# Performance work log

Hardware: AMD Instinct MI355X
Metric: run time of the kernel (lower is better)

Reference implementation:

```python
import jax, jax.numpy as jnp
import numpy as np
import math

B, D, L = 32, 128, 512
NH = 8
DK = D // NH  # 16
DV = D // NH  # 16


def setup_inputs() -> dict:
    key = jax.random.key(0)
    kx, kq, kk, kv, ko = jax.random.split(key, 5)
    # xavier_normal std for [B, Dk, D] slabs: gain*sqrt(2/(fan_in+fan_out)) with fan over last two dims
    std_qkv = math.sqrt(2.0 / (DK + D))
    std_o = math.sqrt(2.0 / (DV * NH + D))
    x = jax.random.normal(kx, (B, D, L), dtype=jnp.float32)
    Wqs = jax.random.normal(kq, (NH, B, DK, D), dtype=jnp.float32) * std_qkv
    Wks = jax.random.normal(kk, (NH, B, DK, D), dtype=jnp.float32) * std_qkv
    Wvs = jax.random.normal(kv, (NH, B, DV, D), dtype=jnp.float32) * std_qkv
    Wo = jax.random.normal(ko, (B, DV * NH, D), dtype=jnp.float32) * std_o
    return {"x": x, "Wqs": Wqs, "Wks": Wks, "Wvs": Wvs, "Wo": Wo}


def reference(x, Wqs, Wks, Wvs, Wo):
    # x: [B, D, L]; Wqs/Wks: [NH, B, DK, D]; Wvs: [NH, B, DV, D]; Wo: [B, DV*NH, D]
    nh, b, dk, d = Wqs.shape
    l = x.shape[-1]
    inv_sqrt_dk = 1.0 / math.sqrt(dk)
    Q = jnp.einsum('nbkd,bdl->nbkl', Wqs, x)  # [NH, B, DK, L]
    K = jnp.einsum('nbkd,bdl->nbkl', Wks, x)  # [NH, B, DK, L]
    V = jnp.einsum('nbvd,bdl->nbvl', Wvs, x)  # [NH, B, DV, L]
    # scores[n,b,l,m] = sum_k Q[n,b,k,l]*K[n,b,k,m]; softmax over l (torch dim=1 of [B,L,L])
    scores = jnp.einsum('nbkl,nbkm->nblm', Q, K) * inv_sqrt_dk
    S = jax.nn.softmax(scores, axis=2)
    heads = jnp.einsum('nbvl,nblm->nbvm', V, S)  # [NH, B, DV, L]
    # .pop() in the original reverses head order before concatenation
    heads = heads[::-1]
    head = heads.transpose(1, 0, 2, 3).reshape(b, nh * heads.shape[2], l)  # [B, NH*DV, L]
    out = jnp.einsum('bod,bdl->bol', Wo, head)  # [B, D, L]
    return out
```

## Files before the change

### kernel.cpp

```cpp
#include <hip/hip_runtime.h>
#include <hip/hip_bf16.h>
#include <math.h>

#define B_   32
#define D_   128
#define L_   512
#define NH_  8
#define DK_  16

#define QKS  24
#define VST  520
#define XST  40

#define LOG2E 1.4426950408889634f
#define QSC   (0.25f * LOG2E)
#define SH2   (-11.541560327111707f)

typedef _Float16 h2 __attribute__((ext_vector_type(2)));
typedef _Float16 h4 __attribute__((ext_vector_type(4)));
typedef _Float16 h8 __attribute__((ext_vector_type(8)));
typedef __attribute__((ext_vector_type(4)))  float f32x4;
typedef __attribute__((ext_vector_type(16))) float f32x16;
typedef unsigned int u32x2 __attribute__((ext_vector_type(2)));
typedef unsigned int u32x4 __attribute__((ext_vector_type(4)));

__device__ __forceinline__ unsigned int cvt_pk_u(float a, float b) {
    return __builtin_bit_cast(unsigned int, __builtin_amdgcn_cvt_pkrtz(a, b));
}

#define MFMA_K32(a, b, c) __builtin_amdgcn_mfma_f32_16x16x32_f16((a), (b), (c), 0, 0, 0)
#define MFMA_32(a, b, c)  __builtin_amdgcn_mfma_f32_32x32x16_f16((a), (b), (c), 0, 0, 0)

__global__ __launch_bounds__(512, 2) void attn_mfma(
    const float* __restrict__ x,
    const float* __restrict__ Wq,
    const float* __restrict__ Wk,
    const float* __restrict__ Wv,
    _Float16* __restrict__ Ht)
{
    __shared__ __attribute__((aligned(16))) _Float16 T32[512 * XST];
    __shared__ __attribute__((aligned(16))) _Float16 Qh[512 * QKS];
    __shared__ __attribute__((aligned(16))) _Float16 Kh[512 * QKS];
    __shared__ __attribute__((aligned(16))) _Float16 Vs[32 * VST];

    const int nb = blockIdx.x;
    const int n  = nb >> 5;
    const int b  = nb & 31;
    const int t  = threadIdx.x;
    const int wv = t >> 6;
    const int ln = t & 63;
    const int l16 = ln & 15;
    const int g4  = ln >> 4;
    const int lm  = ln & 31;
    const int hi  = ln >> 5;

    const float* xb = x + (size_t)b * D_ * L_;
    const size_t woff = (size_t)(n * B_ + b) * DK_ * D_;
    const float* pWq = Wq + woff;
    const float* pWk = Wk + woff;
    const float* pWv = Wv + woff;

    {
        const h8 ones8 = {(_Float16)1.f,(_Float16)1.f,(_Float16)1.f,(_Float16)1.f,
                          (_Float16)1.f,(_Float16)1.f,(_Float16)1.f,(_Float16)1.f};
        #pragma unroll
        for (int i = 0; i < 2; ++i) {
            const int c = t + i * 512;
            const int row = 16 + (c >> 6), cc = (c & 63) * 8;
            *(h8*)&Vs[row * VST + cc] = ones8;
        }
    }

    const int sdd = (t >> 7) * 8;
    const int sl0 = (t & 127) * 4;

    f32x4 Qa[4], Ka[4], Va[4];
    #pragma unroll
    for (int lt = 0; lt < 4; ++lt) {
        Qa[lt] = (f32x4){0.f,0.f,0.f,0.f};
        Ka[lt] = (f32x4){0.f,0.f,0.f,0.f};
        Va[lt] = (f32x4){0.f,0.f,0.f,0.f};
    }

    for (int ks = 0; ks < 4; ++ks) {
        {
            f32x4 xv[8];
            #pragma unroll
            for (int j = 0; j < 8; ++j)
                xv[j] = *(const f32x4*)&xb[(size_t)(ks * 32 + sdd + j) * L_ + sl0];
            #pragma unroll
            for (int i = 0; i < 4; ++i) {
                h8 w;
                #pragma unroll
                for (int j = 0; j < 8; ++j) w[j] = (_Float16)xv[j][i];
                *(h8*)&T32[(sl0 + i) * XST + sdd] = w;
            }
        }
        __syncthreads();

        const int d0 = ks * 32 + g4 * 8;
        const float* aq = pWq + l16 * D_ + d0;
        const float* ak = pWk + l16 * D_ + d0;
        const float* av = pWv + l16 * D_ + d0;
        const f32x4 q0 = *(const f32x4*)aq, q1 = *(const f32x4*)(aq + 4);
        const f32x4 k0 = *(const f32x4*)ak, k1 = *(const f32x4*)(ak + 4);
        const f32x4 v0 = *(const f32x4*)av, v1 = *(const f32x4*)(av + 4);
        h8 Aq, Ak, Av;
        #pragma unroll
        for (int j = 0; j < 4; ++j) {
            Aq[j] = (_Float16)q0[j]; Aq[j + 4] = (_Float16)q1[j];
            Ak[j] = (_Float16)k0[j]; Ak[j + 4] = (_Float16)k1[j];
            Av[j] = (_Float16)v0[j]; Av[j + 4] = (_Float16)v1[j];
        }
        #pragma unroll
        for (int lt = 0; lt < 4; ++lt) {
            const int l = wv * 64 + lt * 16 + l16;
            const h8 Bx = *(const h8*)&T32[l * XST + g4 * 8];
            Qa[lt] = MFMA_K32(Aq, Bx, Qa[lt]);
            Ka[lt] = MFMA_K32(Ak, Bx, Ka[lt]);
            Va[lt] = MFMA_K32(Av, Bx, Va[lt]);
        }
        __syncthreads();
    }

    #pragma unroll
    for (int lt = 0; lt < 4; ++lt) {
        const int l = wv * 64 + lt * 16 + l16;
        h4 qv, kv;
        #pragma unroll
        for (int r = 0; r < 4; ++r) {
            qv[r] = (_Float16)(Qa[lt][r] * QSC);
            kv[r] = (_Float16)Ka[lt][r];
            Vs[(g4 * 4 + r) * VST + l] = (_Float16)Va[lt][r];
        }
        *(h4*)&Qh[l * QKS + g4 * 4] = qv;
        *(h4*)&Kh[l * QKS + g4 * 4] = kv;
    }
    __syncthreads();

    const int m0 = wv * 64;
    const h8 Bk0 = *(const h8*)&Kh[(m0 + lm) * QKS + 8 * hi];
    const h8 Bk1 = *(const h8*)&Kh[(m0 + 32 + lm) * QKS + 8 * hi];

    f32x16 shiftacc, pv0, pv1;
    #pragma unroll
    for (int i = 0; i < 16; ++i) { shiftacc[i] = SH2; pv0[i] = 0.f; pv1[i] = 0.f; }

    #pragma unroll 2
    for (int t32 = 0; t32 < 16; ++t32) {
        const int lb = t32 * 32;
        const h8 Aq2 = *(const h8*)&Qh[(lb + lm) * QKS + 8 * hi];
        const h8 Bv1 = *(const h8*)&Vs[lm * VST + lb + 8 * hi];
        const h8 Bv2 = *(const h8*)&Vs[lm * VST + lb + 16 + 8 * hi];

        const f32x16 sc0 = MFMA_32(Aq2, Bk0, shiftacc);
        const f32x16 sc1 = MFMA_32(Aq2, Bk1, shiftacc);

        float pA[16], pB[16];
        #pragma unroll
        for (int r = 0; r < 16; ++r) pA[r] = __builtin_amdgcn_exp2f(sc0[r]);
        #pragma unroll
        for (int r = 0; r < 16; ++r) pB[r] = __builtin_amdgcn_exp2f(sc1[r]);

        const unsigned int a0 = cvt_pk_u(pA[0],  pA[1]);
        const unsigned int a1 = cvt_pk_u(pA[2],  pA[3]);
        const unsigned int a2 = cvt_pk_u(pA[4],  pA[5]);
        const unsigned int a3 = cvt_pk_u(pA[6],  pA[7]);
        const unsigned int a4 = cvt_pk_u(pA[8],  pA[9]);
        const unsigned int a5 = cvt_pk_u(pA[10], pA[11]);
        const unsigned int a6 = cvt_pk_u(pA[12], pA[13]);
        const unsigned int a7 = cvt_pk_u(pA[14], pA[15]);
        const unsigned int b0 = cvt_pk_u(pB[0],  pB[1]);
        const unsigned int b1 = cvt_pk_u(pB[2],  pB[3]);
        const unsigned int b2 = cvt_pk_u(pB[4],  pB[5]);
        const unsigned int b3 = cvt_pk_u(pB[6],  pB[7]);
        const unsigned int b4 = cvt_pk_u(pB[8],  pB[9]);
        const unsigned int b5 = cvt_pk_u(pB[10], pB[11]);
        const unsigned int b6 = cvt_pk_u(pB[12], pB[13]);
        const unsigned int b7 = cvt_pk_u(pB[14], pB[15]);

        const u32x2 sA02 = __builtin_amdgcn_permlane32_swap(a0, a2, false, false);
        const u32x2 sA13 = __builtin_amdgcn_permlane32_swap(a1, a3, false, false);
        const u32x2 sA46 = __builtin_amdgcn_permlane32_swap(a4, a6, false, false);
        const u32x2 sA57 = __builtin_amdgcn_permlane32_swap(a5, a7, false, false);
        const u32x2 sB02 = __builtin_amdgcn_permlane32_swap(b0, b2, false, false);
        const u32x2 sB13 = __builtin_amdgcn_permlane32_swap(b1, b3, false, false);
        const u32x2 sB46 = __builtin_amdgcn_permlane32_swap(b4, b6, false, false);
        const u32x2 sB57 = __builtin_amdgcn_permlane32_swap(b5, b7, false, false);
        const h8 A1m0 = __builtin_bit_cast(h8, (u32x4){sA02.x, sA13.x, sA02.y, sA13.y});
        const h8 A2m0 = __builtin_bit_cast(h8, (u32x4){sA46.x, sA57.x, sA46.y, sA57.y});
        const h8 A1m1 = __builtin_bit_cast(h8, (u32x4){sB02.x, sB13.x, sB02.y, sB13.y});
        const h8 A2m1 = __builtin_bit_cast(h8, (u32x4){sB46.x, sB57.x, sB46.y, sB57.y});

        pv0 = MFMA_32(A1m0, Bv1, pv0);
        pv0 = MFMA_32(A2m0, Bv2, pv0);
        pv1 = MFMA_32(A1m1, Bv1, pv1);
        pv1 = MFMA_32(A2m1, Bv2, pv1);
    }

    const int kk = (NH_ - 1 - n) * 16 + l16;
    const int zlane = 16 + 32 * hi;
    _Float16* Hb = Ht + (size_t)b * 512 * 128;
    #pragma unroll
    for (int r = 0; r < 16; ++r) {
        const int mrow = (r & 3) + 8 * (r >> 2) + 4 * hi;
        const float zr0 = __shfl(pv0[r], zlane);
        const float zr1 = __shfl(pv1[r], zlane);
        const float rz0 = __builtin_amdgcn_rcpf(zr0);
        const float rz1 = __builtin_amdgcn_rcpf(zr1);
        if (lm < 16) {
            Hb[(size_t)(m0 + mrow) * 128 + kk]      = (_Float16)(pv0[r] * rz0);
            Hb[(size_t)(m0 + 32 + mrow) * 128 + kk] = (_Float16)(pv1[r] * rz1);
        }
    }
}

__global__ __launch_bounds__(512) void out_proj_mfma(
    const float* __restrict__ Wo,
    const _Float16* __restrict__ Ht,
    float* __restrict__ out)
{
    const int ct = blockIdx.x;
    const int b  = blockIdx.y;
    const int t  = threadIdx.x;
    const int wv = t >> 6;
    const int ln = t & 63;
    const int l16 = ln & 15;
    const int g4  = ln >> 4;

    const float* Wb = Wo + (size_t)b * D_ * D_;
    const _Float16* Hb = Ht + (size_t)b * 512 * 128;

    f32x4 acc[4];
    #pragma unroll
    for (int nt = 0; nt < 4; ++nt) acc[nt] = (f32x4){0.f,0.f,0.f,0.f};

    #pragma unroll
    for (int ks = 0; ks < 4; ++ks) {
        const int k0 = ks * 32 + g4 * 8;
        const float* ap = Wb + (size_t)(wv * 16 + l16) * D_ + k0;
        const f32x4 w0 = *(const f32x4*)ap, w1 = *(const f32x4*)(ap + 4);
        h8 Ah;
        #pragma unroll
        for (int j = 0; j < 4; ++j) {
            Ah[j] = (_Float16)w0[j]; Ah[j + 4] = (_Float16)w1[j];
        }
        #pragma unroll
        for (int nt = 0; nt < 4; ++nt) {
            const h8 Bh = *(const h8*)&Hb[(size_t)(ct * 64 + nt * 16 + l16) * 128 + k0];
            acc[nt] = MFMA_K32(Ah, Bh, acc[nt]);
        }
    }

    float* ob = out + (size_t)b * D_ * L_;
    #pragma unroll
    for (int nt = 0; nt < 4; ++nt) {
        #pragma unroll
        for (int r = 0; r < 4; ++r) {
            ob[(size_t)(wv * 16 + g4 * 4 + r) * L_ + ct * 64 + nt * 16 + l16] = acc[nt][r];
        }
    }
}

extern "C" void kernel_launch(void* const* d_in, const int* in_sizes, int n_in,
                              void* d_out, int out_size, void* d_ws, size_t ws_size,
                              hipStream_t stream)
{
    const float* x  = (const float*)d_in[0];
    const float* Wq = (const float*)d_in[1];
    const float* Wk = (const float*)d_in[2];
    const float* Wv = (const float*)d_in[3];
    const float* Wo = (const float*)d_in[4];
    float* out = (float*)d_out;

    _Float16* Ht = (_Float16*)d_ws;

    attn_mfma<<<dim3(NH_ * B_), dim3(512), 0, stream>>>(x, Wq, Wk, Wv, Ht);
    out_proj_mfma<<<dim3(8, B_), dim3(512), 0, stream>>>(Wo, Ht, out);
}
```

Baseline: 34.95 us.

## Double-buffer x staging, synthesize V ones rows, retile output projection

Splits the x transpose buffer into two shared-memory buffers so the next k-slice's global loads and fp16 conversion overlap the current slice's MFMAs. Removes the constant ones rows from the V shared buffer and substitutes them in registers, shrinking shared memory. The output projection kernel is retiled to 256-thread blocks computing 2x2 MFMA tiles over half as many columns, doubling the block count. This adds shared memory pressure and register use in exchange for hiding load latency.

```diff
diff --git a/kernel.cpp b/kernel.cpp
--- a/kernel.cpp
+++ b/kernel.cpp
@@ -38,10 +38,11 @@
     const float* __restrict__ Wv,
     _Float16* __restrict__ Ht)
 {
-    __shared__ __attribute__((aligned(16))) _Float16 T32[512 * XST];
+    __shared__ __attribute__((aligned(16))) _Float16 T32a[512 * XST];
+    __shared__ __attribute__((aligned(16))) _Float16 T32b[512 * XST];
     __shared__ __attribute__((aligned(16))) _Float16 Qh[512 * QKS];
     __shared__ __attribute__((aligned(16))) _Float16 Kh[512 * QKS];
-    __shared__ __attribute__((aligned(16))) _Float16 Vs[32 * VST];
+    __shared__ __attribute__((aligned(16))) _Float16 Vs[16 * VST];
 
     const int nb = blockIdx.x;
     const int n  = nb >> 5;
@@ -60,19 +61,23 @@
     const float* pWk = Wk + woff;
     const float* pWv = Wv + woff;
 
-    {
-        const h8 ones8 = {(_Float16)1.f,(_Float16)1.f,(_Float16)1.f,(_Float16)1.f,
-                          (_Float16)1.f,(_Float16)1.f,(_Float16)1.f,(_Float16)1.f};
-        #pragma unroll
-        for (int i = 0; i < 2; ++i) {
-            const int c = t + i * 512;
-            const int row = 16 + (c >> 6), cc = (c & 63) * 8;
-            *(h8*)&Vs[row * VST + cc] = ones8;
-        }
-    }
-
     const int sdd = (t >> 7) * 8;
     const int sl0 = (t & 127) * 4;
+
+    #define STAGE(ks_, buf_)                                                   \
+    {                                                                          \
+        f32x4 xv[8];                                                           \
+        _Pragma("unroll")                                                      \
+        for (int j = 0; j < 8; ++j)                                            \
+            xv[j] = *(const f32x4*)&xb[(size_t)((ks_) * 32 + sdd + j) * L_ + sl0]; \
+        _Pragma("unroll")                                                      \
+        for (int i = 0; i < 4; ++i) {                                          \
+            h8 w;                                                              \
+            _Pragma("unroll")                                                  \
+            for (int j = 0; j < 8; ++j) w[j] = (_Float16)xv[j][i];             \
+            *(h8*)&(buf_)[(sl0 + i) * XST + sdd] = w;                          \
+        }                                                                      \
+    }
 
     f32x4 Qa[4], Ka[4], Va[4];
     #pragma unroll
@@ -82,21 +87,14 @@
         Va[lt] = (f32x4){0.f,0.f,0.f,0.f};
     }
 
+    STAGE(0, T32a);
+    __syncthreads();
+
+    #pragma unroll
     for (int ks = 0; ks < 4; ++ks) {
-        {
-            f32x4 xv[8];
-            #pragma unroll
-            for (int j = 0; j < 8; ++j)
-                xv[j] = *(const f32x4*)&xb[(size_t)(ks * 32 + sdd + j) * L_ + sl0];
-            #pragma unroll
-            for (int i = 0; i < 4; ++i) {
-                h8 w;
-                #pragma unroll
-                for (int j = 0; j < 8; ++j) w[j] = (_Float16)xv[j][i];
-                *(h8*)&T32[(sl0 + i) * XST + sdd] = w;
-            }
-        }
-        __syncthreads();
+        _Float16* cur = (ks & 1) ? T32b : T32a;
+        _Float16* nxt = (ks & 1) ? T32a : T32b;
+        if (ks < 3) STAGE(ks + 1, nxt);
 
         const int d0 = ks * 32 + g4 * 8;
         const float* aq = pWq + l16 * D_ + d0;
@@ -115,7 +113,7 @@
         #pragma unroll
         for (int lt = 0; lt < 4; ++lt) {
             const int l = wv * 64 + lt * 16 + l16;
-            const h8 Bx = *(const h8*)&T32[l * XST + g4 * 8];
+            const h8 Bx = *(const h8*)&cur[l * XST + g4 * 8];
             Qa[lt] = MFMA_K32(Aq, Bx, Qa[lt]);
             Ka[lt] = MFMA_K32(Ak, Bx, Ka[lt]);
             Va[lt] = MFMA_K32(Av, Bx, Va[lt]);
@@ -146,12 +144,19 @@
     #pragma unroll
     for (int i = 0; i < 16; ++i) { shiftacc[i] = SH2; pv0[i] = 0.f; pv1[i] = 0.f; }
 
+    const bool vsel = (lm < 16);
+    const int  vrow = lm & 15;
+    const h8 ones8 = {(_Float16)1.f,(_Float16)1.f,(_Float16)1.f,(_Float16)1.f,
+                      (_Float16)1.f,(_Float16)1.f,(_Float16)1.f,(_Float16)1.f};
+
     #pragma unroll 2
     for (int t32 = 0; t32 < 16; ++t32) {
         const int lb = t32 * 32;
-        const h8 Aq2 = *(const h8*)&Qh[(lb + lm) * QKS + 8 * hi];
-        const h8 Bv1 = *(const h8*)&Vs[lm * VST + lb + 8 * hi];
-        const h8 Bv2 = *(const h8*)&Vs[lm * VST + lb + 16 + 8 * hi];
+        const h8 Aq2  = *(const h8*)&Qh[(lb + lm) * QKS + 8 * hi];
+        const h8 Bv1r = *(const h8*)&Vs[vrow * VST + lb + 8 * hi];
+        const h8 Bv2r = *(const h8*)&Vs[vrow * VST + lb + 16 + 8 * hi];
+        const h8 Bv1 = vsel ? Bv1r : ones8;
+        const h8 Bv2 = vsel ? Bv2r : ones8;
 
         const f32x16 sc0 = MFMA_32(Aq2, Bk0, shiftacc);
         const f32x16 sc1 = MFMA_32(Aq2, Bk1, shiftacc);
@@ -215,7 +220,7 @@
     }
 }
 
-__global__ __launch_bounds__(512) void out_proj_mfma(
+__global__ __launch_bounds__(256, 2) void out_proj_mfma(
     const float* __restrict__ Wo,
     const _Float16* __restrict__ Ht,
     float* __restrict__ out)
@@ -227,37 +232,51 @@
     const int ln = t & 63;
     const int l16 = ln & 15;
     const int g4  = ln >> 4;
+    const int col0 = ct * 32;
 
     const float* Wb = Wo + (size_t)b * D_ * D_;
     const _Float16* Hb = Ht + (size_t)b * 512 * 128;
 
-    f32x4 acc[4];
-    #pragma unroll
-    for (int nt = 0; nt < 4; ++nt) acc[nt] = (f32x4){0.f,0.f,0.f,0.f};
+    f32x4 acc[2][2];
+    #pragma unroll
+    for (int mt = 0; mt < 2; ++mt)
+        #pragma unroll
+        for (int nt = 0; nt < 2; ++nt) acc[mt][nt] = (f32x4){0.f,0.f,0.f,0.f};
 
     #pragma unroll
     for (int ks = 0; ks < 4; ++ks) {
         const int k0 = ks * 32 + g4 * 8;
-        const float* ap = Wb + (size_t)(wv * 16 + l16) * D_ + k0;
-        const f32x4 w0 = *(const f32x4*)ap, w1 = *(const f32x4*)(ap + 4);
-        h8 Ah;
-        #pragma unroll
-        for (int j = 0; j < 4; ++j) {
-            Ah[j] = (_Float16)w0[j]; Ah[j + 4] = (_Float16)w1[j];
-        }
-        #pragma unroll
-        for (int nt = 0; nt < 4; ++nt) {
-            const h8 Bh = *(const h8*)&Hb[(size_t)(ct * 64 + nt * 16 + l16) * 128 + k0];
-            acc[nt] = MFMA_K32(Ah, Bh, acc[nt]);
-        }
+        h8 Ah[2];
+        #pragma unroll
+        for (int mt = 0; mt < 2; ++mt) {
+            const float* ap = Wb + (size_t)(wv * 32 + mt * 16 + l16) * D_ + k0;
+            const f32x4 w0 = *(const f32x4*)ap, w1 = *(const f32x4*)(ap + 4);
+            #pragma unroll
+            for (int j = 0; j < 4; ++j) {
+                Ah[mt][j] = (_Float16)w0[j]; Ah[mt][j + 4] = (_Float16)w1[j];
+            }
+        }
+        h8 Bh[2];
+        #pragma unroll
+        for (int nt = 0; nt < 2; ++nt)
+            Bh[nt] = *(const h8*)&Hb[(size_t)(col0 + nt * 16 + l16) * 128 + k0];
+        #pragma unroll
+        for (int mt = 0; mt < 2; ++mt)
+            #pragma unroll
+            for (int nt = 0; nt < 2; ++nt)
+                acc[mt][nt] = MFMA_K32(Ah[mt], Bh[nt], acc[mt][nt]);
     }
 
     float* ob = out + (size_t)b * D_ * L_;
     #pragma unroll
-    for (int nt = 0; nt < 4; ++nt) {
-        #pragma unroll
-        for (int r = 0; r < 4; ++r) {
-            ob[(size_t)(wv * 16 + g4 * 4 + r) * L_ + ct * 64 + nt * 16 + l16] = acc[nt][r];
+    for (int mt = 0; mt < 2; ++mt) {
+        #pragma unroll
+        for (int nt = 0; nt < 2; ++nt) {
+            #pragma unroll
+            for (int r = 0; r < 4; ++r) {
+                ob[(size_t)(wv * 32 + mt * 16 + g4 * 4 + r) * L_ + col0 + nt * 16 + l16]
+                    = acc[mt][nt][r];
+            }
         }
     }
 }
@@ -276,5 +295,5 @@
     _Float16* Ht = (_Float16*)d_ws;
 
     attn_mfma<<<dim3(NH_ * B_), dim3(512), 0, stream>>>(x, Wq, Wk, Wv, Ht);
-    out_proj_mfma<<<dim3(8, B_), dim3(512), 0, stream>>>(Wo, Ht, out);
-}
+    out_proj_mfma<<<dim3(16, B_), dim3(256), 0, stream>>>(Wo, Ht, out);
+}
```

Measured after the change: 34.97 us. About the same (+0.0%).
